# Performance work log

Measured on AMD Instinct MI355X. Metric: run time of the kernel, lower is better.

Reference implementation:

```python
import jax, jax.numpy as jnp
import numpy as np
import math

B = 8
N_SURF_PER, N_LIG_PER = 5000, 128
N_SURF, N_LIG = B * N_SURF_PER, B * N_LIG_PER
N = N_SURF + N_LIG
HID, TDIM, NLAYERS = 512, 64, 6
E_MAX = 131072
RADIUS = 3.5
BOX = 24.1  # box edge so that radius-3.5 cross-degree ~64


def sinusoidal_emb(t, dim):
    # standard SinusoidalPosEmb: cat(sin, cos) over log-spaced freqs
    half = dim // 2
    freqs = jnp.exp(-math.log(10000.0) / (half - 1) * jnp.arange(half, dtype=t.dtype))
    ang = t[:, None] * freqs[None, :]
    return jnp.concatenate([jnp.sin(ang), jnp.cos(ang)], axis=-1)


def setup_inputs() -> dict:
    rng = np.random.default_rng(0)
    surf = rng.uniform(0.0, BOX, (B, N_SURF_PER, 3)).astype(np.float32)
    lig = rng.uniform(0.0, BOX, (B, N_LIG_PER, 3)).astype(np.float32)
    # radius_graph per batch; only surface->ligand edges survive filter_edges,
    # so we materialize exactly the cross edges (others are filtered to weight 0 anyway)
    srcs, dsts = [], []
    for b in range(B):
        d2 = ((surf[b][:, None, :] - lig[b][None, :, :]) ** 2).sum(-1)
        sj, li = np.nonzero(d2 <= RADIUS ** 2)
        srcs.append(b * N_SURF_PER + sj)
        dsts.append(N_SURF + b * N_LIG_PER + li)
    src = np.concatenate(srcs)
    dst = np.concatenate(dsts)
    E = min(len(src), E_MAX)
    edge_index = np.zeros((2, E_MAX), dtype=np.int32)  # pad with (0,0): filtered out
    edge_index[0, :E] = src[:E]
    edge_index[1, :E] = dst[:E]
    batch_surface = np.repeat(np.arange(B), N_SURF_PER).astype(np.int32)
    batch_ligand = np.repeat(np.arange(B), N_LIG_PER).astype(np.int32)

    ks = jax.random.split(jax.random.key(0), 10)

    def gl(k, shp, fan_in):
        return jax.random.normal(k, shp, jnp.float32) / np.sqrt(fan_in)

    return dict(
        surface_pos=jnp.asarray(surf.reshape(-1, 3)),
        init_ligand_pos=jnp.asarray(lig.reshape(-1, 3)),
        time=jax.random.uniform(ks[9], (N_LIG, 1), jnp.float32) * 1000.0,
        edge_index=jnp.asarray(edge_index),
        batch_surface=jnp.asarray(batch_surface),
        batch_ligand=jnp.asarray(batch_ligand),
        W_surf=gl(ks[0], (3, HID), 3), b_surf=jnp.zeros((HID,), jnp.float32),
        W_t1=gl(ks[1], (TDIM, 4 * TDIM), TDIM), b_t1=jnp.zeros((4 * TDIM,), jnp.float32),
        W_t2=gl(ks[2], (4 * TDIM, TDIM), 4 * TDIM), b_t2=jnp.zeros((TDIM,), jnp.float32),
        W_lig=gl(ks[3], (3, HID), 3), b_lig=jnp.zeros((HID,), jnp.float32),
        W_gate=gl(ks[4], (TDIM, HID), TDIM), b_gate=jnp.zeros((HID,), jnp.float32),
        W_hbias=gl(ks[5], (TDIM, HID), TDIM),
        W_gcn=gl(ks[6], (NLAYERS, HID, HID), HID), b_gcn=jnp.zeros((NLAYERS, HID), jnp.float32),
        W_pos=gl(ks[7], (HID, 3), HID), b_pos=jnp.zeros((3,), jnp.float32),
    )


def reference(surface_pos, init_ligand_pos, time, edge_index, batch_surface, batch_ligand,
              W_surf, b_surf, W_t1, b_t1, W_t2, b_t2, W_lig, b_lig,
              W_gate, b_gate, W_hbias, W_gcn, b_gcn, W_pos, b_pos):
    # encoders
    h_surf = surface_pos @ W_surf + b_surf                      # [N_surf, HID]
    t_emb = sinusoidal_emb(jnp.squeeze(time, -1), TDIM)         # [N_lig, TDIM]
    h_time = jax.nn.gelu(t_emb @ W_t1 + b_t1, approximate=False) @ W_t2 + b_t2
    # ConcatSquashLinear: layer(x)*sigmoid(hyper_gate(ctx)) + hyper_bias(ctx)
    h_lig = ((init_ligand_pos @ W_lig + b_lig)
             * jax.nn.sigmoid(h_time @ W_gate + b_gate)
             + h_time @ W_hbias)                                # [N_lig, HID]

    h_node = jnp.concatenate([h_surf, h_lig], axis=0)           # [N, HID]
    mask_ligand = jnp.concatenate([jnp.zeros((N_SURF,), bool), jnp.ones((N_LIG,), bool)])

    src, dst = edge_index[0], edge_index[1]
    # filter_edges: keep surface -> ligand (padded (0,0) edges killed here too)
    w = ((~mask_ligand[src]) & mask_ligand[dst]).astype(h_node.dtype)  # [E]

    # GCN symmetric norm with self loops (edge weight 1 self loop)
    deg = jnp.ones((N,), h_node.dtype).at[dst].add(w)           # in-degree + 1
    dinv = 1.0 / jnp.sqrt(deg)
    norm = w * dinv[src] * dinv[dst]                            # [E]

    # original loop feeds h_node into every layer; only the last output is kept
    for l in range(NLAYERS):
        xw = h_node @ W_gcn[l]                                  # [N, HID]
        msg = jax.ops.segment_sum(norm[:, None] * xw[src], dst, num_segments=N)
        h_combined = msg + (dinv * dinv)[:, None] * xw + b_gcn[l]

    # mask_ligand selects the trailing ligand block (static slice)
    return h_combined[N_SURF:] @ W_pos + b_pos                  # [N_lig, 3]
```

## Files before the change

### kernel.cpp

```cpp
#include <hip/hip_runtime.h>
#include <math.h>

#define N_SURF 40000
#define N_LIG  1024
#define HID    512
#define TDIM   64
#define E_MAX  131072
#define L5     5

#define WS_WP     0
#define WS_A3     1536
#define WS_BSP    1545
#define WS_BPOUT  1548
#define WS_WHBP   1552
#define WS_AGG    1744
#define WS_CNT    4816
#define WS_ZERO_BEGIN 1744
#define WS_ZERO_COUNT 4096

__global__ void k_prep1(const float* __restrict__ Wgcn, const float* __restrict__ Wpos,
                        float* __restrict__ ws) {
    int lane = threadIdx.x & 63;
    int w    = threadIdx.x >> 6;
    int k    = blockIdx.x * 4 + w;
    const float* Wg5 = Wgcn + (size_t)L5 * HID * HID + (size_t)k * HID;
    float a0 = 0.f, a1 = 0.f, a2 = 0.f;
    for (int j = lane; j < HID; j += 64) {
        float v = Wg5[j];
        a0 += v * Wpos[j * 3 + 0];
        a1 += v * Wpos[j * 3 + 1];
        a2 += v * Wpos[j * 3 + 2];
    }
    for (int m = 32; m; m >>= 1) {
        a0 += __shfl_xor(a0, m);
        a1 += __shfl_xor(a1, m);
        a2 += __shfl_xor(a2, m);
    }
    if (lane == 0) {
        ws[WS_WP + k * 3 + 0] = a0;
        ws[WS_WP + k * 3 + 1] = a1;
        ws[WS_WP + k * 3 + 2] = a2;
    }
    int idx = blockIdx.x * blockDim.x + threadIdx.x;
    if (idx < WS_ZERO_COUNT) ws[WS_ZERO_BEGIN + idx] = 0.f;
}

__global__ __launch_bounds__(256) void k_mid(
    const float* __restrict__ Wsurf, const float* __restrict__ bsurf,
    const float* __restrict__ bgcn,  const float* __restrict__ Wpos,
    const float* __restrict__ bpos,  const float* __restrict__ Whb,
    const int*   __restrict__ ei,    const float* __restrict__ spos,
    float* __restrict__ ws) {
    if (blockIdx.x < 52) {
        int lane = threadIdx.x & 63;
        int w    = threadIdx.x >> 6;
        int o    = blockIdx.x * 4 + w;
        if (o >= 207) return;
        float acc = 0.f;
        if (o < 9) {
            int a = o / 3, jp = o - a * 3;
            for (int k = lane; k < HID; k += 64)
                acc += Wsurf[a * HID + k] * ws[WS_WP + k * 3 + jp];
        } else if (o < 12) {
            int jp = o - 9;
            for (int k = lane; k < HID; k += 64)
                acc += bsurf[k] * ws[WS_WP + k * 3 + jp];
        } else if (o < 15) {
            int jp = o - 12;
            for (int j = lane; j < HID; j += 64)
                acc += bgcn[L5 * HID + j] * Wpos[j * 3 + jp];
        } else {
            int r = (o - 15) / 3, jp = (o - 15) % 3;
            for (int j = lane; j < HID; j += 64)
                acc += Whb[r * HID + j] * ws[WS_WP + j * 3 + jp];
        }
        for (int m = 32; m; m >>= 1) acc += __shfl_xor(acc, m);
        if (lane == 0) {
            if (o < 9)        ws[WS_A3 + o] = acc;
            else if (o < 12)  ws[WS_BSP + (o - 9)] = acc;
            else if (o < 15)  ws[WS_BPOUT + (o - 12)] = acc + bpos[o - 12];
            else              ws[WS_WHBP + (o - 15)] = acc;
        }
    } else {
        int e = (blockIdx.x - 52) * 256 + threadIdx.x;
        int s = ei[e];
        int d = ei[E_MAX + e];
        if (s < N_SURF && d >= N_SURF) {
            int li = d - N_SURF;
            atomicAdd(&ws[WS_AGG + li * 3 + 0], spos[s * 3 + 0]);
            atomicAdd(&ws[WS_AGG + li * 3 + 1], spos[s * 3 + 1]);
            atomicAdd(&ws[WS_AGG + li * 3 + 2], spos[s * 3 + 2]);
            atomicAdd(&ws[WS_CNT + li], 1.0f);
        }
    }
}

__global__ __launch_bounds__(256, 4) void k_lig(
    const float* __restrict__ lpos,  const float* __restrict__ tarr,
    const float* __restrict__ Wt1,   const float* __restrict__ bt1,
    const float* __restrict__ Wt2,   const float* __restrict__ bt2,
    const float* __restrict__ Wlig,  const float* __restrict__ blig,
    const float* __restrict__ Wgate, const float* __restrict__ bgate,
    const float* __restrict__ ws,    float* __restrict__ out)
{
    __shared__ float s_emb[4][64];
    __shared__ float s_h1[4][256];
    __shared__ float s_ht[4][64];
    __shared__ float s_out[4][4][3];
    int t    = threadIdx.x;
    int lane = t & 63;
    int w    = t >> 6;
    int i0   = blockIdx.x * 4;

    {
        float tt = tarr[i0 + w];
        const float coef = -0.29710775f;
        float ang = tt * expf(coef * (float)(lane & 31));
        s_emb[w][lane] = (lane < 32) ? sinf(ang) : cosf(ang);
    }
    __syncthreads();
    {
        float b = bt1[t];
        float acc[4] = {b, b, b, b};
        #pragma unroll 16
        for (int k = 0; k < 64; ++k) {
            float wv = Wt1[k * 256 + t];
            #pragma unroll
            for (int n = 0; n < 4; ++n) acc[n] += s_emb[n][k] * wv;
        }
        #pragma unroll
        for (int n = 0; n < 4; ++n)
            s_h1[n][t] = 0.5f * acc[n] * (1.f + erff(acc[n] * 0.70710678f));
    }
    __syncthreads();
    {
        float a0 = 0.f, a1 = 0.f, a2 = 0.f, a3 = 0.f;
        #pragma unroll 16
        for (int k = 0; k < 256; k += 4) {
            a0 += s_h1[w][k + 0] * Wt2[(k + 0) * 64 + lane];
            a1 += s_h1[w][k + 1] * Wt2[(k + 1) * 64 + lane];
            a2 += s_h1[w][k + 2] * Wt2[(k + 2) * 64 + lane];
            a3 += s_h1[w][k + 3] * Wt2[(k + 3) * 64 + lane];
        }
        s_ht[w][lane] = bt2[lane] + ((a0 + a1) + (a2 + a3));
    }
    __syncthreads();

    float px[4], py[4], pz[4];
    #pragma unroll
    for (int n = 0; n < 4; ++n) {
        px[n] = lpos[(i0 + n) * 3 + 0];
        py[n] = lpos[(i0 + n) * 3 + 1];
        pz[n] = lpos[(i0 + n) * 3 + 2];
    }
    float a[4][3] = {};
    #pragma unroll
    for (int r = 0; r < 2; ++r) {
        int j = r * 256 + t;
        float bg = bgate[j];
        float g[4] = {bg, bg, bg, bg};
        #pragma unroll 16
        for (int k = 0; k < 64; ++k) {
            float wv = Wgate[k * 512 + j];
            #pragma unroll
            for (int n = 0; n < 4; ++n) g[n] += s_ht[n][k] * wv;
        }
        float wl0 = Wlig[j], wl1 = Wlig[512 + j], wl2 = Wlig[1024 + j], bl = blig[j];
        float wp0 = ws[WS_WP + j * 3 + 0];
        float wp1 = ws[WS_WP + j * 3 + 1];
        float wp2 = ws[WS_WP + j * 3 + 2];
        #pragma unroll
        for (int n = 0; n < 4; ++n) {
            float p  = bl + px[n] * wl0 + py[n] * wl1 + pz[n] * wl2;
            float hl = p * (1.f / (1.f + expf(-g[n])));
            a[n][0] += hl * wp0;
            a[n][1] += hl * wp1;
            a[n][2] += hl * wp2;
        }
    }
    if (t < 64) {
        float h0 = ws[WS_WHBP + t * 3 + 0];
        float h1v = ws[WS_WHBP + t * 3 + 1];
        float h2 = ws[WS_WHBP + t * 3 + 2];
        #pragma unroll
        for (int n = 0; n < 4; ++n) {
            float ht = s_ht[n][t];
            a[n][0] += ht * h0;
            a[n][1] += ht * h1v;
            a[n][2] += ht * h2;
        }
    }
    #pragma unroll
    for (int n = 0; n < 4; ++n)
        #pragma unroll
        for (int jp = 0; jp < 3; ++jp)
            for (int m = 32; m; m >>= 1) a[n][jp] += __shfl_xor(a[n][jp], m);
    if (lane == 0)
        #pragma unroll
        for (int n = 0; n < 4; ++n)
            #pragma unroll
            for (int jp = 0; jp < 3; ++jp) s_out[w][n][jp] = a[n][jp];
    __syncthreads();
    if (t < 4) {
        int n = t, i = i0 + n;
        float d  = ws[WS_CNT + i];
        float s1 = 1.f / sqrtf(1.f + d);
        float s2 = 1.f / (1.f + d);
        float c  = s1 * d;
        float ax = s1 * ws[WS_AGG + i * 3 + 0];
        float ay = s1 * ws[WS_AGG + i * 3 + 1];
        float az = s1 * ws[WS_AGG + i * 3 + 2];
        #pragma unroll
        for (int jp = 0; jp < 3; ++jp) {
            float b = s_out[0][n][jp] + s_out[1][n][jp] + s_out[2][n][jp] + s_out[3][n][jp];
            out[i * 3 + jp] = ax * ws[WS_A3 + 0 + jp] +
                              ay * ws[WS_A3 + 3 + jp] +
                              az * ws[WS_A3 + 6 + jp] +
                              c  * ws[WS_BSP + jp]    +
                              s2 * b                  +
                              ws[WS_BPOUT + jp];
        }
    }
}

extern "C" void kernel_launch(void* const* d_in, const int* in_sizes, int n_in,
                              void* d_out, int out_size, void* d_ws, size_t ws_size,
                              hipStream_t stream) {
    const float* spos  = (const float*)d_in[0];
    const float* lpos  = (const float*)d_in[1];
    const float* tarr  = (const float*)d_in[2];
    const int*   ei    = (const int*)  d_in[3];
    const float* Wsurf = (const float*)d_in[6];
    const float* bsurf = (const float*)d_in[7];
    const float* Wt1   = (const float*)d_in[8];
    const float* bt1   = (const float*)d_in[9];
    const float* Wt2   = (const float*)d_in[10];
    const float* bt2   = (const float*)d_in[11];
    const float* Wlig  = (const float*)d_in[12];
    const float* blig  = (const float*)d_in[13];
    const float* Wgate = (const float*)d_in[14];
    const float* bgate = (const float*)d_in[15];
    const float* Whb   = (const float*)d_in[16];
    const float* Wgcn  = (const float*)d_in[17];
    const float* bgcn  = (const float*)d_in[18];
    const float* Wpos  = (const float*)d_in[19];
    const float* bpos  = (const float*)d_in[20];
    float* ws  = (float*)d_ws;
    float* out = (float*)d_out;

    hipLaunchKernelGGL(k_prep1, dim3(128), dim3(256), 0, stream, Wgcn, Wpos, ws);
    hipLaunchKernelGGL(k_mid,   dim3(52 + E_MAX / 256), dim3(256), 0, stream,
                       Wsurf, bsurf, bgcn, Wpos, bpos, Whb, ei, spos, ws);
    hipLaunchKernelGGL(k_lig,   dim3(N_LIG / 4), dim3(256), 0, stream,
                       lpos, tarr, Wt1, bt1, Wt2, bt2, Wlig, blig, Wgate, bgate, ws, out);
}
```

Measured before the change: 38.24 us.

## Fuse three kernels into one persistent kernel with software grid barriers

Merges the prep, mid and ligand kernels into a single 256-block kernel that synchronises across the grid with atomic-counter barriers. Independent work (the time MLP, Wgcn·Wpos and workspace zeroing) runs before the first barrier, and the gate and projection work overlaps before the second. The aim is to remove two kernel-launch gaps and inter-kernel dependency latency. In exchange it adds a memset launch for the barrier counters, relies on all 256 blocks being co-resident, and runs the edge scatter on fewer threads.

Result: slower. 141.4 us (+269.9%).

```diff
diff --git a/kernel.cpp b/kernel.cpp
--- a/kernel.cpp
+++ b/kernel.cpp
@@ -4,9 +4,9 @@
 #define N_SURF 40000
 #define N_LIG  1024
 #define HID    512
-#define TDIM   64
 #define E_MAX  131072
 #define L5     5
+#define NBLK   256
 
 #define WS_WP     0
 #define WS_A3     1536
@@ -17,72 +17,105 @@
 #define WS_CNT    4816
 #define WS_ZERO_BEGIN 1744
 #define WS_ZERO_COUNT 4096
-
-__global__ void k_prep1(const float* __restrict__ Wgcn, const float* __restrict__ Wpos,
-                        float* __restrict__ ws) {
-    int lane = threadIdx.x & 63;
-    int w    = threadIdx.x >> 6;
-    int k    = blockIdx.x * 4 + w;
-    const float* Wg5 = Wgcn + (size_t)L5 * HID * HID + (size_t)k * HID;
-    float a0 = 0.f, a1 = 0.f, a2 = 0.f;
-    for (int j = lane; j < HID; j += 64) {
-        float v = Wg5[j];
-        a0 += v * Wpos[j * 3 + 0];
-        a1 += v * Wpos[j * 3 + 1];
-        a2 += v * Wpos[j * 3 + 2];
-    }
-    for (int m = 32; m; m >>= 1) {
-        a0 += __shfl_xor(a0, m);
-        a1 += __shfl_xor(a1, m);
-        a2 += __shfl_xor(a2, m);
-    }
-    if (lane == 0) {
-        ws[WS_WP + k * 3 + 0] = a0;
-        ws[WS_WP + k * 3 + 1] = a1;
-        ws[WS_WP + k * 3 + 2] = a2;
-    }
-    int idx = blockIdx.x * blockDim.x + threadIdx.x;
-    if (idx < WS_ZERO_COUNT) ws[WS_ZERO_BEGIN + idx] = 0.f;
+#define WS_BAR    5840
+
+__device__ __forceinline__ void gridbar(unsigned* cnt) {
+    __threadfence();
+    __syncthreads();
+    if (threadIdx.x == 0) {
+        atomicAdd(cnt, 1u);
+        while (__hip_atomic_load(cnt, __ATOMIC_ACQUIRE, __HIP_MEMORY_SCOPE_AGENT) < NBLK) {}
+    }
+    __syncthreads();
+    __threadfence();
 }
 
-__global__ __launch_bounds__(256) void k_mid(
+__global__ __launch_bounds__(256) void k_fused(
+    const float* __restrict__ Wgcn,  const float* __restrict__ Wpos,
     const float* __restrict__ Wsurf, const float* __restrict__ bsurf,
-    const float* __restrict__ bgcn,  const float* __restrict__ Wpos,
-    const float* __restrict__ bpos,  const float* __restrict__ Whb,
+    const float* __restrict__ bgcn,  const float* __restrict__ bpos,
+    const float* __restrict__ Whb,
     const int*   __restrict__ ei,    const float* __restrict__ spos,
-    float* __restrict__ ws) {
-    if (blockIdx.x < 52) {
-        int lane = threadIdx.x & 63;
-        int w    = threadIdx.x >> 6;
-        int o    = blockIdx.x * 4 + w;
-        if (o >= 207) return;
-        float acc = 0.f;
-        if (o < 9) {
-            int a = o / 3, jp = o - a * 3;
-            for (int k = lane; k < HID; k += 64)
-                acc += Wsurf[a * HID + k] * ws[WS_WP + k * 3 + jp];
-        } else if (o < 12) {
-            int jp = o - 9;
-            for (int k = lane; k < HID; k += 64)
-                acc += bsurf[k] * ws[WS_WP + k * 3 + jp];
-        } else if (o < 15) {
-            int jp = o - 12;
-            for (int j = lane; j < HID; j += 64)
-                acc += bgcn[L5 * HID + j] * Wpos[j * 3 + jp];
-        } else {
-            int r = (o - 15) / 3, jp = (o - 15) % 3;
-            for (int j = lane; j < HID; j += 64)
-                acc += Whb[r * HID + j] * ws[WS_WP + j * 3 + jp];
-        }
-        for (int m = 32; m; m >>= 1) acc += __shfl_xor(acc, m);
+    const float* __restrict__ lpos,  const float* __restrict__ tarr,
+    const float* __restrict__ Wt1,   const float* __restrict__ bt1,
+    const float* __restrict__ Wt2,   const float* __restrict__ bt2,
+    const float* __restrict__ Wlig,  const float* __restrict__ blig,
+    const float* __restrict__ Wgate, const float* __restrict__ bgate,
+    float* __restrict__ ws,          float* __restrict__ out)
+{
+    __shared__ float s_emb[4][64];
+    __shared__ float s_h1[4][256];
+    __shared__ float s_ht[4][64];
+    __shared__ float s_out[4][4][3];
+    unsigned* bar = (unsigned*)(ws + WS_BAR);
+    int t    = threadIdx.x;
+    int lane = t & 63;
+    int w    = t >> 6;
+    int b    = blockIdx.x;
+    int i0   = b * 4;
+
+    if (w < 2) {
+        int row = b * 2 + w;
+        const float* Wg5 = Wgcn + (size_t)L5 * HID * HID + (size_t)row * HID;
+        float a0 = 0.f, a1 = 0.f, a2 = 0.f;
+        for (int j = lane; j < HID; j += 64) {
+            float v = Wg5[j];
+            a0 += v * Wpos[j * 3 + 0];
+            a1 += v * Wpos[j * 3 + 1];
+            a2 += v * Wpos[j * 3 + 2];
+        }
+        for (int m = 32; m; m >>= 1) {
+            a0 += __shfl_xor(a0, m);
+            a1 += __shfl_xor(a1, m);
+            a2 += __shfl_xor(a2, m);
+        }
         if (lane == 0) {
-            if (o < 9)        ws[WS_A3 + o] = acc;
-            else if (o < 12)  ws[WS_BSP + (o - 9)] = acc;
-            else if (o < 15)  ws[WS_BPOUT + (o - 12)] = acc + bpos[o - 12];
-            else              ws[WS_WHBP + (o - 15)] = acc;
+            ws[WS_WP + row * 3 + 0] = a0;
+            ws[WS_WP + row * 3 + 1] = a1;
+            ws[WS_WP + row * 3 + 2] = a2;
         }
     } else {
-        int e = (blockIdx.x - 52) * 256 + threadIdx.x;
+        int idx = b * 128 + (t - 128);
+        if (idx < WS_ZERO_COUNT) ws[WS_ZERO_BEGIN + idx] = 0.f;
+    }
+
+    {
+        float tt = tarr[i0 + w];
+        const float coef = -0.29710775f;
+        float ang = tt * expf(coef * (float)(lane & 31));
+        s_emb[w][lane] = (lane < 32) ? sinf(ang) : cosf(ang);
+    }
+    __syncthreads();
+    {
+        float bb = bt1[t];
+        float acc[4] = {bb, bb, bb, bb};
+        #pragma unroll 16
+        for (int k = 0; k < 64; ++k) {
+            float wv = Wt1[k * 256 + t];
+            #pragma unroll
+            for (int n = 0; n < 4; ++n) acc[n] += s_emb[n][k] * wv;
+        }
+        #pragma unroll
+        for (int n = 0; n < 4; ++n)
+            s_h1[n][t] = 0.5f * acc[n] * (1.f + erff(acc[n] * 0.70710678f));
+    }
+    __syncthreads();
+    {
+        float a0 = 0.f, a1 = 0.f, a2 = 0.f, a3 = 0.f;
+        #pragma unroll 16
+        for (int k = 0; k < 256; k += 4) {
+            a0 += s_h1[w][k + 0] * Wt2[(k + 0) * 64 + lane];
+            a1 += s_h1[w][k + 1] * Wt2[(k + 1) * 64 + lane];
+            a2 += s_h1[w][k + 2] * Wt2[(k + 2) * 64 + lane];
+            a3 += s_h1[w][k + 3] * Wt2[(k + 3) * 64 + lane];
+        }
+        s_ht[w][lane] = bt2[lane] + ((a0 + a1) + (a2 + a3));
+    }
+    gridbar(&bar[0]);
+
+    #pragma unroll
+    for (int rep = 0; rep < 2; ++rep) {
+        int e = rep * (E_MAX / 2) + b * 256 + t;
         int s = ei[e];
         int d = ei[E_MAX + e];
         if (s < N_SURF && d >= N_SURF) {
@@ -93,59 +126,36 @@
             atomicAdd(&ws[WS_CNT + li], 1.0f);
         }
     }
-}
-
-__global__ __launch_bounds__(256, 4) void k_lig(
-    const float* __restrict__ lpos,  const float* __restrict__ tarr,
-    const float* __restrict__ Wt1,   const float* __restrict__ bt1,
-    const float* __restrict__ Wt2,   const float* __restrict__ bt2,
-    const float* __restrict__ Wlig,  const float* __restrict__ blig,
-    const float* __restrict__ Wgate, const float* __restrict__ bgate,
-    const float* __restrict__ ws,    float* __restrict__ out)
-{
-    __shared__ float s_emb[4][64];
-    __shared__ float s_h1[4][256];
-    __shared__ float s_ht[4][64];
-    __shared__ float s_out[4][4][3];
-    int t    = threadIdx.x;
-    int lane = t & 63;
-    int w    = t >> 6;
-    int i0   = blockIdx.x * 4;
-
-    {
-        float tt = tarr[i0 + w];
-        const float coef = -0.29710775f;
-        float ang = tt * expf(coef * (float)(lane & 31));
-        s_emb[w][lane] = (lane < 32) ? sinf(ang) : cosf(ang);
-    }
-    __syncthreads();
-    {
-        float b = bt1[t];
-        float acc[4] = {b, b, b, b};
-        #pragma unroll 16
-        for (int k = 0; k < 64; ++k) {
-            float wv = Wt1[k * 256 + t];
-            #pragma unroll
-            for (int n = 0; n < 4; ++n) acc[n] += s_emb[n][k] * wv;
-        }
-        #pragma unroll
-        for (int n = 0; n < 4; ++n)
-            s_h1[n][t] = 0.5f * acc[n] * (1.f + erff(acc[n] * 0.70710678f));
-    }
-    __syncthreads();
-    {
-        float a0 = 0.f, a1 = 0.f, a2 = 0.f, a3 = 0.f;
-        #pragma unroll 16
-        for (int k = 0; k < 256; k += 4) {
-            a0 += s_h1[w][k + 0] * Wt2[(k + 0) * 64 + lane];
-            a1 += s_h1[w][k + 1] * Wt2[(k + 1) * 64 + lane];
-            a2 += s_h1[w][k + 2] * Wt2[(k + 2) * 64 + lane];
-            a3 += s_h1[w][k + 3] * Wt2[(k + 3) * 64 + lane];
-        }
-        s_ht[w][lane] = bt2[lane] + ((a0 + a1) + (a2 + a3));
-    }
-    __syncthreads();
-
+    if (b < 52) {
+        int o = b * 4 + w;
+        if (o < 207) {
+            float acc = 0.f;
+            if (o < 9) {
+                int a = o / 3, jp = o - a * 3;
+                for (int k = lane; k < HID; k += 64)
+                    acc += Wsurf[a * HID + k] * ws[WS_WP + k * 3 + jp];
+            } else if (o < 12) {
+                int jp = o - 9;
+                for (int k = lane; k < HID; k += 64)
+                    acc += bsurf[k] * ws[WS_WP + k * 3 + jp];
+            } else if (o < 15) {
+                int jp = o - 12;
+                for (int j = lane; j < HID; j += 64)
+                    acc += bgcn[L5 * HID + j] * Wpos[j * 3 + jp];
+            } else {
+                int r = (o - 15) / 3, jp = (o - 15) % 3;
+                for (int j = lane; j < HID; j += 64)
+                    acc += Whb[r * HID + j] * ws[WS_WP + j * 3 + jp];
+            }
+            for (int m = 32; m; m >>= 1) acc += __shfl_xor(acc, m);
+            if (lane == 0) {
+                if (o < 9)        ws[WS_A3 + o] = acc;
+                else if (o < 12)  ws[WS_BSP + (o - 9)] = acc;
+                else if (o < 15)  ws[WS_BPOUT + (o - 12)] = acc + bpos[o - 12];
+                else              ws[WS_WHBP + (o - 15)] = acc;
+            }
+        }
+    }
     float px[4], py[4], pz[4];
     #pragma unroll
     for (int n = 0; n < 4; ++n) {
@@ -178,10 +188,12 @@
             a[n][2] += hl * wp2;
         }
     }
+    gridbar(&bar[1]);
+
     if (t < 64) {
-        float h0 = ws[WS_WHBP + t * 3 + 0];
+        float h0  = ws[WS_WHBP + t * 3 + 0];
         float h1v = ws[WS_WHBP + t * 3 + 1];
-        float h2 = ws[WS_WHBP + t * 3 + 2];
+        float h2  = ws[WS_WHBP + t * 3 + 2];
         #pragma unroll
         for (int n = 0; n < 4; ++n) {
             float ht = s_ht[n][t];
@@ -212,12 +224,12 @@
         float az = s1 * ws[WS_AGG + i * 3 + 2];
         #pragma unroll
         for (int jp = 0; jp < 3; ++jp) {
-            float b = s_out[0][n][jp] + s_out[1][n][jp] + s_out[2][n][jp] + s_out[3][n][jp];
+            float bb = s_out[0][n][jp] + s_out[1][n][jp] + s_out[2][n][jp] + s_out[3][n][jp];
             out[i * 3 + jp] = ax * ws[WS_A3 + 0 + jp] +
                               ay * ws[WS_A3 + 3 + jp] +
                               az * ws[WS_A3 + 6 + jp] +
                               c  * ws[WS_BSP + jp]    +
-                              s2 * b                  +
+                              s2 * bb                 +
                               ws[WS_BPOUT + jp];
         }
     }
@@ -248,9 +260,10 @@
     float* ws  = (float*)d_ws;
     float* out = (float*)d_out;
 
-    hipLaunchKernelGGL(k_prep1, dim3(128), dim3(256), 0, stream, Wgcn, Wpos, ws);
-    hipLaunchKernelGGL(k_mid,   dim3(52 + E_MAX / 256), dim3(256), 0, stream,
-                       Wsurf, bsurf, bgcn, Wpos, bpos, Whb, ei, spos, ws);
-    hipLaunchKernelGGL(k_lig,   dim3(N_LIG / 4), dim3(256), 0, stream,
-                       lpos, tarr, Wt1, bt1, Wt2, bt2, Wlig, blig, Wgate, bgate, ws, out);
+    hipMemsetAsync((char*)d_ws + WS_BAR * sizeof(float), 0, 2 * sizeof(unsigned), stream);
+
+    hipLaunchKernelGGL(k_fused, dim3(NBLK), dim3(256), 0, stream,
+                       Wgcn, Wpos, Wsurf, bsurf, bgcn, bpos, Whb,
+                       ei, spos, lpos, tarr, Wt1, bt1, Wt2, bt2,
+                       Wlig, blig, Wgate, bgate, ws, out);
 }
```
